# Performance work log

Hardware: AMD Instinct MI355X
Metric: run time of the kernel (lower is better)

Reference implementation:

```python
import jax, jax.numpy as jnp
import numpy as np

B, N, CI, CO = 2, 64, 32, 32  # batch, n points, Rs_in channels (j), Rs_out channels (i)


def setup_inputs() -> dict:
    key = jax.random.key(0)
    kf, kg, kw = jax.random.split(key, 3)
    features = jax.random.normal(kf, (B, N, N, CI), dtype=jnp.float32)
    geometry = jax.random.normal(kg, (B, N, 3), dtype=jnp.float32)
    # Continuous kernel parameters: linear map from relative vector (xyz) to 6*CO*CI kernel entries
    W = jax.random.normal(kw, (3, 6 * CO * CI), dtype=jnp.float32) / jnp.sqrt(3.0)
    return {"features": features, "geometry": geometry, "W": W, "n_norm": 1}


def reference(features, geometry, W, n_norm):
    z, n = geometry.shape[:2]
    ci = features.shape[-1]
    co = W.shape[1] // (6 * ci)
    # rel[z, a, b] = r_b - r_a  (rb = unsqueeze(1), ra = unsqueeze(2))
    rel = geometry[:, None, :, :] - geometry[:, :, None, :]  # [z, a, b, 3]
    k = jnp.einsum('zabx,xk->zabk', rel, W).reshape(z, n, n, 6 * co, ci)
    k = k / jnp.sqrt(6.0 * (n_norm ** 2))
    k1, k2, k3, k4, k5, k6 = jnp.split(k, 6, axis=3)  # each [z, a, b, i, j]
    # Precompute shared feature reductions over c and d once (fused HBM savings)
    fs = features.sum(axis=2)   # sum over d -> [z, c, j]
    fd = features.sum(axis=1)   # sum over c -> [z, d, j]
    ft = fs.sum(axis=1)         # sum over c,d -> [z, j]
    out = jnp.einsum('zabij,zj->zabi', k1, ft)
    out = out + jnp.einsum('zacij,zcj->zai', k2, fs)[:, :, None, :]
    out = out + jnp.einsum('zadij,zdj->zai', k3, fd)[:, :, None, :]
    out = out + jnp.einsum('zbcij,zcj->zbi', k4, fs)[:, None, :, :]
    out = out + jnp.einsum('zbdij,zdj->zbi', k5, fd)[:, None, :, :]
    out = out + jnp.einsum('zcdij,zcdj->zi', k6, features)[:, None, None, :]
    return out  # [z, a, b, i]
```

## Files before the change

kernel.cpp:

```cpp
#include <hip/hip_runtime.h>
#include <math.h>

#define NZ 2
#define NN 64
#define NCI 32
#define NCO 32

#define WS_PART 0
#define WS_QA   14336
#define WS_QB   14528
#define WS_GAM  14720

__global__ __launch_bounds__(256) void k_reduce(const float* __restrict__ feat,
                                                const float* __restrict__ geom,
                                                float* __restrict__ part) {
    const int bid = blockIdx.x;
    const int z = bid >> 5;
    const int s = bid & 31;
    const int tid = threadIdx.x;
    const int j = tid & 31;
    const int grp = tid >> 5;

    __shared__ float gsh[NN * 3];
    __shared__ float red[8][7][32];

    if (tid < NN * 3) gsh[tid] = geom[z * NN * 3 + tid];
    __syncthreads();

    float ft = 0.f;
    float a0 = 0.f, a1 = 0.f, a2 = 0.f;
    float b0 = 0.f, b1 = 0.f, b2 = 0.f;

    const float* fz = feat + (size_t)z * NN * NN * NCI;
    const int p0 = s * 128 + grp * 16;
    #pragma unroll 4
    for (int t = 0; t < 16; ++t) {
        const int p = p0 + t;
        const float f = fz[p * NCI + j];
        const int c = p >> 6;
        const int d = p & 63;
        const float gc0 = gsh[c * 3 + 0], gc1 = gsh[c * 3 + 1], gc2 = gsh[c * 3 + 2];
        const float gd0 = gsh[d * 3 + 0], gd1 = gsh[d * 3 + 1], gd2 = gsh[d * 3 + 2];
        ft += f;
        a0 = fmaf(gc0, f, a0); a1 = fmaf(gc1, f, a1); a2 = fmaf(gc2, f, a2);
        b0 = fmaf(gd0, f, b0); b1 = fmaf(gd1, f, b1); b2 = fmaf(gd2, f, b2);
    }

    red[grp][0][j] = ft;
    red[grp][1][j] = a0; red[grp][2][j] = a1; red[grp][3][j] = a2;
    red[grp][4][j] = b0; red[grp][5][j] = b1; red[grp][6][j] = b2;
    __syncthreads();

    if (tid < 7 * 32) {
        const int q = tid >> 5, jj = tid & 31;
        float sum = 0.f;
        #pragma unroll
        for (int g = 0; g < 8; ++g) sum += red[g][q][jj];
        part[((z * 32 + s) * 7 + q) * 32 + jj] = sum;
    }
}

__global__ __launch_bounds__(128) void k_coeff(const float* __restrict__ part,
                                               const float* __restrict__ W,
                                               const int* __restrict__ nnp,
                                               float* __restrict__ QA,
                                               float* __restrict__ QB,
                                               float* __restrict__ gam) {
    const int z = blockIdx.x;
    const int tid = threadIdx.x;

    __shared__ float acc[7][32];
    __shared__ float gred[3][32];

    for (int idx = tid; idx < 7 * 32; idx += 128) {
        const int q = idx >> 5, j = idx & 31;
        float sum = 0.f;
        for (int s = 0; s < 32; ++s)
            sum += part[((z * 32 + s) * 7 + q) * 32 + j];
        acc[q][j] = sum;
    }
    __syncthreads();

    const int v = *nnp;
    const float nn = (v > 0 && v < (1 << 23)) ? (float)v : __int_as_float(v);
    const float scale = 1.0f / sqrtf(6.0f * nn * nn);

    if (tid < 96) {
        const int x = tid >> 5;
        const int i = tid & 31;
        const float* Wp = W + x * 6 * NCO * NCI;
        float q1 = 0.f, q23 = 0.f, q45 = 0.f, gp = 0.f;
        for (int j = 0; j < 32; ++j) {
            const float ftj = acc[0][j];
            const float gsj = acc[1 + x][j];
            const float gdj = acc[4 + x][j];
            const float w0 = Wp[0 * 1024 + i * 32 + j];
            const float w1 = Wp[1 * 1024 + i * 32 + j];
            const float w2 = Wp[2 * 1024 + i * 32 + j];
            const float w3 = Wp[3 * 1024 + i * 32 + j];
            const float w4 = Wp[4 * 1024 + i * 32 + j];
            const float w5 = Wp[5 * 1024 + i * 32 + j];
            q1  = fmaf(w0, ftj, q1);
            q23 = fmaf(w1 + w2, ftj, q23);
            q45 = fmaf(w3 + w4, ftj, q45);
            gp  = fmaf(w1 + w3 - w5, gsj, gp);
            gp  = fmaf(w2 + w4 + w5, gdj, gp);
        }
        QA[(z * 3 + x) * 32 + i] = scale * (q1 + q23);
        QB[(z * 3 + x) * 32 + i] = scale * (q1 - q45);
        gred[x][i] = gp;
    }
    __syncthreads();

    if (tid < 32) {
        gam[z * 32 + tid] = scale * (gred[0][tid] + gred[1][tid] + gred[2][tid]);
    }
}

__global__ __launch_bounds__(256) void k_out(const float* __restrict__ geom,
                                             const float* __restrict__ QA,
                                             const float* __restrict__ QB,
                                             const float* __restrict__ gam,
                                             float* __restrict__ out, int total) {
    const int idx = blockIdx.x * 256 + threadIdx.x;
    if (idx >= total) return;
    const int i = idx & 31;
    const int b = (idx >> 5) & 63;
    const int a = (idx >> 11) & 63;
    const int z = idx >> 17;

    const float* gz = geom + z * NN * 3;
    float r = gam[z * 32 + i];
    #pragma unroll
    for (int x = 0; x < 3; ++x) {
        r = fmaf(gz[b * 3 + x], QB[(z * 3 + x) * 32 + i], r);
        r = fmaf(-gz[a * 3 + x], QA[(z * 3 + x) * 32 + i], r);
    }
    out[idx] = r;
}

extern "C" void kernel_launch(void* const* d_in, const int* in_sizes, int n_in,
                              void* d_out, int out_size, void* d_ws, size_t ws_size,
                              hipStream_t stream) {
    const float* feat = (const float*)d_in[0];
    const float* geom = (const float*)d_in[1];
    const float* W    = (const float*)d_in[2];
    const int*   nnp  = (const int*)d_in[3];

    float* ws   = (float*)d_ws;
    float* part = ws + WS_PART;
    float* QA   = ws + WS_QA;
    float* QB   = ws + WS_QB;
    float* gam  = ws + WS_GAM;
    float* out  = (float*)d_out;

    k_reduce<<<NZ * 32, 256, 0, stream>>>(feat, geom, part);
    k_coeff<<<NZ, 128, 0, stream>>>(part, W, nnp, QA, QB, gam);

    const int total = out_size;
    k_out<<<(total + 255) / 256, 256, 0, stream>>>(geom, QA, QB, gam, out, total);
}
```

Measured before the change: 17.67 us.

## Fuse coefficient kernel into output kernel and vectorize loads and stores

Merges the two-block coefficient kernel into the output kernel: every output block now recomputes the per-batch QA/QB/gamma coefficients from the partial sums and W. This removes one kernel launch and the global round trip for the coefficients. The reduce kernel and the output writes also switch to float4 accesses with 4 channels per thread. The cost is redundant coefficient work (partial-sum reduction plus a W matvec) repeated in each of 256 blocks, with extra syncthreads before any output is written.

```diff
diff --git a/kernel.cpp b/kernel.cpp
--- a/kernel.cpp
+++ b/kernel.cpp
@@ -6,10 +6,12 @@
 #define NCI 32
 #define NCO 32
 
-#define WS_PART 0
-#define WS_QA   14336
-#define WS_QB   14528
-#define WS_GAM  14720
+#define PART_Z_STRIDE (32 * 7 * 32)
+
+__device__ __forceinline__ void ld4(const float* __restrict__ p, float* d) {
+    const float4 v = *(const float4*)p;
+    d[0] = v.x; d[1] = v.y; d[2] = v.z; d[3] = v.w;
+}
 
 __global__ __launch_bounds__(256) void k_reduce(const float* __restrict__ feat,
                                                 const float* __restrict__ geom,
@@ -18,65 +20,83 @@
     const int z = bid >> 5;
     const int s = bid & 31;
     const int tid = threadIdx.x;
-    const int j = tid & 31;
-    const int grp = tid >> 5;
+    const int cg = tid & 7;
+    const int rg = tid >> 3;
 
     __shared__ float gsh[NN * 3];
-    __shared__ float red[8][7][32];
+    __shared__ float red[32][7][32];
 
     if (tid < NN * 3) gsh[tid] = geom[z * NN * 3 + tid];
     __syncthreads();
 
-    float ft = 0.f;
-    float a0 = 0.f, a1 = 0.f, a2 = 0.f;
-    float b0 = 0.f, b1 = 0.f, b2 = 0.f;
+    float ft[4] = {0.f, 0.f, 0.f, 0.f};
+    float As[3][4] = {{0.f}};
+    float Ad[3][4] = {{0.f}};
 
     const float* fz = feat + (size_t)z * NN * NN * NCI;
-    const int p0 = s * 128 + grp * 16;
-    #pragma unroll 4
-    for (int t = 0; t < 16; ++t) {
+    const int p0 = s * 128 + rg * 4;
+    #pragma unroll
+    for (int t = 0; t < 4; ++t) {
         const int p = p0 + t;
-        const float f = fz[p * NCI + j];
+        float f[4];
+        ld4(fz + (size_t)p * NCI + cg * 4, f);
         const int c = p >> 6;
         const int d = p & 63;
-        const float gc0 = gsh[c * 3 + 0], gc1 = gsh[c * 3 + 1], gc2 = gsh[c * 3 + 2];
-        const float gd0 = gsh[d * 3 + 0], gd1 = gsh[d * 3 + 1], gd2 = gsh[d * 3 + 2];
-        ft += f;
-        a0 = fmaf(gc0, f, a0); a1 = fmaf(gc1, f, a1); a2 = fmaf(gc2, f, a2);
-        b0 = fmaf(gd0, f, b0); b1 = fmaf(gd1, f, b1); b2 = fmaf(gd2, f, b2);
+        float gc[3], gd[3];
+        #pragma unroll
+        for (int x = 0; x < 3; ++x) { gc[x] = gsh[c * 3 + x]; gd[x] = gsh[d * 3 + x]; }
+        #pragma unroll
+        for (int k = 0; k < 4; ++k) {
+            ft[k] += f[k];
+            #pragma unroll
+            for (int x = 0; x < 3; ++x) {
+                As[x][k] = fmaf(gc[x], f[k], As[x][k]);
+                Ad[x][k] = fmaf(gd[x], f[k], Ad[x][k]);
+            }
+        }
     }
 
-    red[grp][0][j] = ft;
-    red[grp][1][j] = a0; red[grp][2][j] = a1; red[grp][3][j] = a2;
-    red[grp][4][j] = b0; red[grp][5][j] = b1; red[grp][6][j] = b2;
+    const int j0 = cg * 4;
+    #pragma unroll
+    for (int k = 0; k < 4; ++k) {
+        red[rg][0][j0 + k] = ft[k];
+        #pragma unroll
+        for (int x = 0; x < 3; ++x) {
+            red[rg][1 + x][j0 + k] = As[x][k];
+            red[rg][4 + x][j0 + k] = Ad[x][k];
+        }
+    }
     __syncthreads();
 
     if (tid < 7 * 32) {
         const int q = tid >> 5, jj = tid & 31;
         float sum = 0.f;
         #pragma unroll
-        for (int g = 0; g < 8; ++g) sum += red[g][q][jj];
-        part[((z * 32 + s) * 7 + q) * 32 + jj] = sum;
+        for (int g = 0; g < 32; ++g) sum += red[g][q][jj];
+        part[(size_t)z * PART_Z_STRIDE + (s * 7 + q) * 32 + jj] = sum;
     }
 }
 
-__global__ __launch_bounds__(128) void k_coeff(const float* __restrict__ part,
-                                               const float* __restrict__ W,
-                                               const int* __restrict__ nnp,
-                                               float* __restrict__ QA,
-                                               float* __restrict__ QB,
-                                               float* __restrict__ gam) {
-    const int z = blockIdx.x;
+__global__ __launch_bounds__(256) void k_out(const float* __restrict__ part,
+                                             const float* __restrict__ W,
+                                             const float* __restrict__ geom,
+                                             const int* __restrict__ nnp,
+                                             float* __restrict__ out) {
+    const int z = blockIdx.x >> 7;
     const int tid = threadIdx.x;
 
+    __shared__ float gsh[NN * 3];
     __shared__ float acc[7][32];
-    __shared__ float gred[3][32];
+    __shared__ float sQA[3][32], sQB[3][32], gred[3][32], sgam[32];
 
-    for (int idx = tid; idx < 7 * 32; idx += 128) {
-        const int q = idx >> 5, j = idx & 31;
+    if (tid < NN * 3) gsh[tid] = geom[z * NN * 3 + tid];
+
+    if (tid < 7 * 32) {
+        const int q = tid >> 5, j = tid & 31;
+        const float* pz = part + (size_t)z * PART_Z_STRIDE;
         float sum = 0.f;
-        for (int s = 0; s < 32; ++s)
-            sum += part[((z * 32 + s) * 7 + q) * 32 + j];
+        #pragma unroll 8
+        for (int sl = 0; sl < 32; ++sl) sum += pz[(sl * 7 + q) * 32 + j];
         acc[q][j] = sum;
     }
     __syncthreads();
@@ -88,55 +108,53 @@
     if (tid < 96) {
         const int x = tid >> 5;
         const int i = tid & 31;
-        const float* Wp = W + x * 6 * NCO * NCI;
+        const float* Wp = W + x * 6 * NCO * NCI + i * NCI;
         float q1 = 0.f, q23 = 0.f, q45 = 0.f, gp = 0.f;
-        for (int j = 0; j < 32; ++j) {
-            const float ftj = acc[0][j];
-            const float gsj = acc[1 + x][j];
-            const float gdj = acc[4 + x][j];
-            const float w0 = Wp[0 * 1024 + i * 32 + j];
-            const float w1 = Wp[1 * 1024 + i * 32 + j];
-            const float w2 = Wp[2 * 1024 + i * 32 + j];
-            const float w3 = Wp[3 * 1024 + i * 32 + j];
-            const float w4 = Wp[4 * 1024 + i * 32 + j];
-            const float w5 = Wp[5 * 1024 + i * 32 + j];
-            q1  = fmaf(w0, ftj, q1);
-            q23 = fmaf(w1 + w2, ftj, q23);
-            q45 = fmaf(w3 + w4, ftj, q45);
-            gp  = fmaf(w1 + w3 - w5, gsj, gp);
-            gp  = fmaf(w2 + w4 + w5, gdj, gp);
+        #pragma unroll 2
+        for (int j4 = 0; j4 < 8; ++j4) {
+            float w[6][4];
+            #pragma unroll
+            for (int m = 0; m < 6; ++m) ld4(Wp + m * 1024 + j4 * 4, w[m]);
+            #pragma unroll
+            for (int k = 0; k < 4; ++k) {
+                const int j = j4 * 4 + k;
+                const float ftj = acc[0][j];
+                const float gsj = acc[1 + x][j];
+                const float gdj = acc[4 + x][j];
+                q1  = fmaf(w[0][k], ftj, q1);
+                q23 = fmaf(w[1][k] + w[2][k], ftj, q23);
+                q45 = fmaf(w[3][k] + w[4][k], ftj, q45);
+                gp  = fmaf(w[1][k] + w[3][k] - w[5][k], gsj, gp);
+                gp  = fmaf(w[2][k] + w[4][k] + w[5][k], gdj, gp);
+            }
         }
-        QA[(z * 3 + x) * 32 + i] = scale * (q1 + q23);
-        QB[(z * 3 + x) * 32 + i] = scale * (q1 - q45);
+        sQA[x][i] = scale * (q1 + q23);
+        sQB[x][i] = scale * (q1 - q45);
         gred[x][i] = gp;
     }
     __syncthreads();
+    if (tid < 32) sgam[tid] = scale * (gred[0][tid] + gred[1][tid] + gred[2][tid]);
+    __syncthreads();
 
-    if (tid < 32) {
-        gam[z * 32 + tid] = scale * (gred[0][tid] + gred[1][tid] + gred[2][tid]);
-    }
-}
+    const int i0 = (tid & 7) * 4;
+    const int ab = ((blockIdx.x & 127) << 5) + (tid >> 3);
+    const int a = ab >> 6, b = ab & 63;
 
-__global__ __launch_bounds__(256) void k_out(const float* __restrict__ geom,
-                                             const float* __restrict__ QA,
-                                             const float* __restrict__ QB,
-                                             const float* __restrict__ gam,
-                                             float* __restrict__ out, int total) {
-    const int idx = blockIdx.x * 256 + threadIdx.x;
-    if (idx >= total) return;
-    const int i = idx & 31;
-    const int b = (idx >> 5) & 63;
-    const int a = (idx >> 11) & 63;
-    const int z = idx >> 17;
-
-    const float* gz = geom + z * NN * 3;
-    float r = gam[z * 32 + i];
+    float r[4];
+    #pragma unroll
+    for (int k = 0; k < 4; ++k) r[k] = sgam[i0 + k];
     #pragma unroll
     for (int x = 0; x < 3; ++x) {
-        r = fmaf(gz[b * 3 + x], QB[(z * 3 + x) * 32 + i], r);
-        r = fmaf(-gz[a * 3 + x], QA[(z * 3 + x) * 32 + i], r);
+        const float gb = gsh[b * 3 + x];
+        const float ga = gsh[a * 3 + x];
+        #pragma unroll
+        for (int k = 0; k < 4; ++k) {
+            r[k] = fmaf(gb, sQB[x][i0 + k], r[k]);
+            r[k] = fmaf(-ga, sQA[x][i0 + k], r[k]);
+        }
     }
-    out[idx] = r;
+    float4 o; o.x = r[0]; o.y = r[1]; o.z = r[2]; o.w = r[3];
+    *(float4*)(out + ((size_t)(z * 4096 + ab)) * 32 + i0) = o;
 }
 
 extern "C" void kernel_launch(void* const* d_in, const int* in_sizes, int n_in,
@@ -147,16 +165,9 @@
     const float* W    = (const float*)d_in[2];
     const int*   nnp  = (const int*)d_in[3];
 
-    float* ws   = (float*)d_ws;
-    float* part = ws + WS_PART;
-    float* QA   = ws + WS_QA;
-    float* QB   = ws + WS_QB;
-    float* gam  = ws + WS_GAM;
+    float* part = (float*)d_ws;
     float* out  = (float*)d_out;
 
     k_reduce<<<NZ * 32, 256, 0, stream>>>(feat, geom, part);
-    k_coeff<<<NZ, 128, 0, stream>>>(part, W, nnp, QA, QB, gam);
-
-    const int total = out_size;
-    k_out<<<(total + 255) / 256, 256, 0, stream>>>(geom, QA, QB, gam, out, total);
+    k_out<<<NZ * 128, 256, 0, stream>>>(part, W, geom, nnp, out);
 }
```

New measurement: 17.25 us. 2.4% less time.
